# Performance work log

Hardware: AMD Instinct MI355X
Metric: run time of the kernel (lower is better)

Reference implementation:

```python
import jax, jax.numpy as jnp
import numpy as np

D_IN_NUM = 16
D_IN_CAT = 16
D_OUT = 10
DIM = 512
N_FREQ = 32
FREQ_SCALE = 0.01
D_EMB = 48
TEMP = 1.0
CHUNK = 5000


def setup_inputs() -> dict:
    key = jax.random.key(0)
    ks = jax.random.split(key, 10)
    B, N = 1024, 40000
    d_in_total = D_IN_NUM * D_EMB + D_IN_CAT
    return {
        "x_num": jax.random.uniform(ks[0], (B, D_IN_NUM), dtype=jnp.float32),
        "x_cat": jax.random.uniform(ks[1], (B, D_IN_CAT), dtype=jnp.float32),
        "y": jax.random.randint(ks[2], (B,), 0, D_OUT),
        "candidate_x_num": jax.random.uniform(ks[3], (N, D_IN_NUM), dtype=jnp.float32),
        "candidate_x_cat": jax.random.uniform(ks[4], (N, D_IN_CAT), dtype=jnp.float32),
        "candidate_y": jax.random.randint(ks[5], (N,), 0, D_OUT),
        "frequencies": FREQ_SCALE * jax.random.normal(ks[6], (D_IN_NUM, N_FREQ), dtype=jnp.float32),
        "lin_w": 0.05 * jax.random.normal(ks[7], (2 * N_FREQ, D_EMB), dtype=jnp.float32),
        "lin_b": jnp.zeros((D_EMB,), dtype=jnp.float32),
        "enc_w": 0.02 * jax.random.normal(ks[8], (d_in_total, DIM), dtype=jnp.float32),
        "enc_b": jnp.zeros((DIM,), dtype=jnp.float32),
    }


def _plr_encode(x_num, x_cat, frequencies, lin_w, lin_b, enc_w, enc_b):
    # PLR 'lite' embedding: [B, F] -> [B, F, 2*n_freq] -> [B, F, d_emb]
    t = 2.0 * jnp.pi * frequencies[None] * x_num[:, :, None]        # [B,F,n_freq]
    feats = jnp.concatenate([jnp.cos(t), jnp.sin(t)], axis=-1)       # [B,F,2n_freq]
    emb = jax.nn.relu(feats @ lin_w + lin_b)                         # [B,F,d_emb]
    flat = emb.reshape(emb.shape[0], -1)                             # [B,F*d_emb]
    h = jnp.concatenate([flat, x_cat], axis=1) @ enc_w + enc_b       # [B,dim]
    return h


def reference(x_num, x_cat, y, candidate_x_num, candidate_x_cat, candidate_y,
              frequencies, lin_w, lin_b, enc_w, enc_b):
    q = _plr_encode(x_num, x_cat, frequencies, lin_w, lin_b, enc_w, enc_b)           # [B,dim]
    c = _plr_encode(candidate_x_num, candidate_x_cat, frequencies, lin_w, lin_b, enc_w, enc_b)  # [N,dim]
    cand_y = jax.nn.one_hot(candidate_y, D_OUT, dtype=jnp.float32)                   # [N,K]

    # pairwise Euclidean distance (matmul form, as torch.cdist)
    d2 = (jnp.sum(q * q, axis=1, keepdims=True)
          + jnp.sum(c * c, axis=1)[None, :]
          - 2.0 * q @ c.T)
    dist = jnp.sqrt(jnp.maximum(d2, 1e-12)) / TEMP                                   # [B,N]
    exp_d = jnp.exp(-dist)                                                           # [B,N]

    # original accumulates per-5000-chunk logsumexp of exp(-d) additively
    B, N = exp_d.shape
    n_chunks = N // CHUNK
    lse = jax.nn.logsumexp(exp_d.reshape(B, n_chunks, CHUNK), axis=-1).sum(axis=-1)  # [B]
    logits = exp_d @ cand_y                                                          # [B,K]
    return jnp.log(logits) - lse[:, None]
```

## Files before the change

### kernel.cpp

```cpp
#include <hip/hip_runtime.h>
#include <math.h>

typedef __attribute__((ext_vector_type(8))) short bf16x8;
typedef __attribute__((ext_vector_type(4))) float f32x4;
typedef unsigned short u16;
typedef unsigned int u32;

#define BQ 1024
#define NCAND 40000
#define ROWS_TOT 41024
#define NF 16
#define NFREQ 32
#define DEMB 48
#define KDIM 800
#define ASTRIDE 808
#define DIM 512
#define NCLS 10
#define NCHUNK 8
#define CHUNKSZ 5000
#define CT_PER_CHUNK 40
#define NCT 320
#define PSTRIDE 136
#define MROWS 64
#define TWO_PI 6.28318530717958647692f

__device__ __forceinline__ u16 f2bf(float f) {
  u32 u = __float_as_uint(f);
  u32 r = u + 0x7fffu + ((u >> 16) & 1u);
  return (u16)(r >> 16);
}
__device__ __forceinline__ float bf2f(u16 b) { return __uint_as_float(((u32)b) << 16); }
__device__ __forceinline__ u32 cvt_pk_bf16(float lo, float hi) {
  u32 r;
  asm("v_cvt_pk_bf16_f32 %0, %1, %2" : "=v"(r) : "v"(lo), "v"(hi));
  return r;
}

__global__ __launch_bounds__(256)
void k_prep(const float* __restrict__ enc_w, u16* __restrict__ enc_wT)
{
  int idx = blockIdx.x * 256 + threadIdx.x;
  if (idx >= DIM * KDIM) return;
  int n = idx / KDIM, k = idx - n * KDIM;
  u16 v = 0;
  if (k < 784) v = f2bf(enc_w[k * DIM + n]);
  enc_wT[idx] = v;
}

__global__ __launch_bounds__(512, 2)
void k_encode(const float* __restrict__ xq_num, const float* __restrict__ xq_cat,
              const float* __restrict__ xc_num, const float* __restrict__ xc_cat,
              const float* __restrict__ freq, const float* __restrict__ lin_w,
              const float* __restrict__ lin_b, const u16* __restrict__ enc_wT,
              const float* __restrict__ enc_b,
              u16* __restrict__ h_bf, float* __restrict__ norms)
{
  __shared__ u16 a_s[MROWS * ASTRIDE];
  __shared__ float norm_s[MROWS];

  const int t = threadIdx.x;
  const int row0 = blockIdx.x * MROWS;
  const bool isq = (row0 < BQ);
  const float* __restrict__ xnum = isq ? xq_num : xc_num;
  const float* __restrict__ xcat = isq ? xq_cat : xc_cat;
  const int rbase = isq ? row0 : (row0 - BQ);

  const int wid = t >> 6, l = t & 63, hi = l >> 4, lo = l & 15;

  if (t < MROWS) norm_s[t] = 0.f;
  for (int i = t; i < MROWS * 16; i += 512) {
    int r = i >> 4, c = i & 15;
    a_s[r * ASTRIDE + 768 + c] = f2bf(xcat[(rbase + r) * NF + c]);
  }
  for (int i = t; i < MROWS * 24; i += 512) {
    int r = i / 24, c = i - r * 24;
    a_s[r * ASTRIDE + 784 + c] = 0;
  }

  {
    float fq[8];
    *(float4*)&fq[0] = *(const float4*)&freq[lo * NFREQ + hi * 8];
    *(float4*)&fq[4] = *(const float4*)&freq[lo * NFREQ + hi * 8 + 4];
    float xv[8];
#pragma unroll
    for (int mi = 0; mi < 8; ++mi)
      xv[mi] = xnum[(rbase + wid * 8 + mi) * NF + lo];

    bf16x8 lwb[2][3];
#pragma unroll
    for (int kf = 0; kf < 2; ++kf)
#pragma unroll
      for (int nf = 0; nf < 3; ++nf)
#pragma unroll
        for (int e = 0; e < 8; ++e)
          lwb[kf][nf][e] = (short)f2bf(lin_w[(kf * 32 + hi * 8 + e) * DEMB + nf * 16 + lo]);
    float lb[3];
#pragma unroll
    for (int nf = 0; nf < 3; ++nf) lb[nf] = lin_b[nf * 16 + lo];

#pragma unroll
    for (int mi = 0; mi < 8; ++mi) {
      bf16x8 ac, as_;
#pragma unroll
      for (int e = 0; e < 8; ++e) {
        float tt = TWO_PI * fq[e] * xv[mi];
        ac[e] = (short)f2bf(__cosf(tt));
        as_[e] = (short)f2bf(__sinf(tt));
      }
#pragma unroll
      for (int nf = 0; nf < 3; ++nf) {
        f32x4 ec = {0.f, 0.f, 0.f, 0.f};
        ec = __builtin_amdgcn_mfma_f32_16x16x32_bf16(ac, lwb[0][nf], ec, 0, 0, 0);
        ec = __builtin_amdgcn_mfma_f32_16x16x32_bf16(as_, lwb[1][nf], ec, 0, 0, 0);
#pragma unroll
        for (int reg = 0; reg < 4; ++reg) {
          int f = hi * 4 + reg;
          int r = wid * 8 + mi;
          float v = fmaxf(ec[reg] + lb[nf], 0.f);
          a_s[r * ASTRIDE + f * DEMB + nf * 16 + lo] = f2bf(v);
        }
      }
    }
  }
  __syncthreads();

  f32x4 acc[4][4];
#pragma unroll
  for (int mf = 0; mf < 4; ++mf)
#pragma unroll
    for (int nf = 0; nf < 4; ++nf) acc[mf][nf] = 0.f;

  const u16* bwbase = enc_wT + (size_t)(wid * 64 + lo) * KDIM + hi * 8;
  const u16* asbase = a_s + lo * ASTRIDE + hi * 8;

  bf16x8 afA[4], bwA[4], afB[4], bwB[4];

#define LOADK(kt, af, bw)                                                     \
  {                                                                           \
    _Pragma("unroll")                                                         \
    for (int nf = 0; nf < 4; ++nf)                                            \
      bw[nf] = *(const bf16x8*)(bwbase + (size_t)nf * 16 * KDIM + (kt) * 32); \
    _Pragma("unroll")                                                         \
    for (int mf = 0; mf < 4; ++mf)                                            \
      af[mf] = *(const bf16x8*)(asbase + mf * 16 * ASTRIDE + (kt) * 32);      \
  }
#define MFMAK(af, bw)                                                         \
  {                                                                           \
    _Pragma("unroll")                                                         \
    for (int mf = 0; mf < 4; ++mf)                                            \
      _Pragma("unroll")                                                       \
      for (int nf = 0; nf < 4; ++nf)                                          \
        acc[mf][nf] =                                                         \
            __builtin_amdgcn_mfma_f32_16x16x32_bf16(af[mf], bw[nf],           \
                                                    acc[mf][nf], 0, 0, 0);    \
  }

  LOADK(0, afA, bwA);
#pragma unroll
  for (int i = 0; i < 12; ++i) {
    LOADK(2 * i + 1, afB, bwB);
    MFMAK(afA, bwA);
    LOADK(2 * i + 2, afA, bwA);
    MFMAK(afB, bwB);
  }
  MFMAK(afA, bwA);
#undef LOADK
#undef MFMAK

  float encb_v[4];
#pragma unroll
  for (int nf = 0; nf < 4; ++nf) encb_v[nf] = enc_b[wid * 64 + nf * 16 + lo];
  float nacc[4][4];
#pragma unroll
  for (int mf = 0; mf < 4; ++mf)
#pragma unroll
    for (int r = 0; r < 4; ++r) nacc[mf][r] = 0.f;

#pragma unroll
  for (int mf = 0; mf < 4; ++mf)
#pragma unroll
    for (int nf = 0; nf < 4; ++nf)
#pragma unroll
      for (int r = 0; r < 4; ++r) {
        int m = mf * 16 + hi * 4 + r;
        int n = wid * 64 + nf * 16 + lo;
        float hv = acc[mf][nf][r] + encb_v[nf];
        u16 ub = f2bf(hv);
        h_bf[(size_t)(row0 + m) * DIM + n] = ub;
        float hb = bf2f(ub);
        nacc[mf][r] = fmaf(hb, hb, nacc[mf][r]);
      }
#pragma unroll
  for (int mf = 0; mf < 4; ++mf)
#pragma unroll
    for (int r = 0; r < 4; ++r) {
      float v = nacc[mf][r];
      v += __shfl_xor(v, 1); v += __shfl_xor(v, 2);
      v += __shfl_xor(v, 4); v += __shfl_xor(v, 8);
      if (lo == 0) atomicAdd(&norm_s[mf * 16 + hi * 4 + r], v);
    }
  __syncthreads();
  if (t < MROWS) norms[row0 + t] = norm_s[t];
}

__global__ __launch_bounds__(256)
void k_dist(const u16* __restrict__ h_bf, const float* __restrict__ norms,
            const int* __restrict__ cand_y,
            float* __restrict__ cls_part, float* __restrict__ lse_part)
{
  __shared__ __align__(16) u16 AB_s[32768];
  __shared__ float qn_s[128];
  __shared__ float cn_s[128];
  __shared__ int cy_s[128];
  __shared__ float lse_s[128];

  u16* P_s = AB_s;

  const int flat = blockIdx.x;
  const int xcd = flat & 7;
  const int i = flat >> 3;
  const int ct = xcd * CT_PER_CHUNK + (i >> 3);
  const int qt = i & 7;

  const int t = threadIdx.x;
  const int chunk = xcd;
  const int ctl = ct - chunk * CT_PER_CHUNK;
  const int cand0 = chunk * CHUNKSZ + ctl * 128;
  const int cend = chunk * CHUNKSZ + CHUNKSZ;
  const int q0 = qt * 128;

  if (t < 128) {
    lse_s[t] = 0.f;
    qn_s[t] = norms[q0 + t];
    int j = cand0 + t; if (j > cend - 1) j = cend - 1;
    cn_s[t] = norms[BQ + j];
    cy_s[t] = cand_y[j];
  }

  const int wid = t >> 6, l = t & 63, hi = l >> 4, lo = l & 15;
  const int wc = wid & 1, wq = wid >> 1;

#define STAGE(dstoff, kt)                                                      \
  {                                                                            \
    _Pragma("unroll")                                                          \
    for (int p = 0; p < 4; ++p) {                                              \
      int seg = wid * 4 + p;                                                   \
      int lrow = seg * 8 + (l >> 3);                                           \
      int scol = ((l & 7) * 16) ^ ((lrow & 7) << 4);                           \
      int crow = cand0 + lrow; if (crow > cend - 1) crow = cend - 1;           \
      const u16* srcA = h_bf + (size_t)(BQ + crow) * DIM + (kt) * 64 + (scol >> 1); \
      __builtin_amdgcn_global_load_lds(                                        \
          (const __attribute__((address_space(1))) u32*)srcA,                  \
          (__attribute__((address_space(3))) u32*)(AB_s + (dstoff) + seg * 512), \
          16, 0, 0);                                                           \
      const u16* srcB = h_bf + (size_t)(q0 + lrow) * DIM + (kt) * 64 + (scol >> 1); \
      __builtin_amdgcn_global_load_lds(                                        \
          (const __attribute__((address_space(1))) u32*)srcB,                  \
          (__attribute__((address_space(3))) u32*)(AB_s + (dstoff) + 8192 + seg * 512), \
          16, 0, 0);                                                           \
    }                                                                          \
  }

  f32x4 acc[4][4];
#pragma unroll
  for (int mi = 0; mi < 4; ++mi)
#pragma unroll
    for (int ni = 0; ni < 4; ++ni) acc[mi][ni] = 0.f;

  STAGE(0, 0);
  STAGE(16384, 1);

#pragma unroll
  for (int kt = 0; kt < 8; ++kt) {
    if (kt == 7) asm volatile("s_waitcnt vmcnt(0)" ::: "memory");
    else         asm volatile("s_waitcnt vmcnt(8)" ::: "memory");
    __builtin_amdgcn_s_barrier();
    __builtin_amdgcn_sched_barrier(0);

    const u16* Ac = AB_s + (kt & 1) * 16384;
    const u16* Bc = Ac + 8192;
#pragma unroll
    for (int ks = 0; ks < 2; ++ks) {
      bf16x8 af[4], bq[4];
#pragma unroll
      for (int mi = 0; mi < 4; ++mi) {
        int row = wc * 64 + mi * 16 + lo;
        int byt = (hi * 16 + ks * 64) ^ ((row & 7) << 4);
        af[mi] = *(const bf16x8*)&Ac[row * 64 + (byt >> 1)];
      }
#pragma unroll
      for (int ni = 0; ni < 4; ++ni) {
        int row = wq * 64 + ni * 16 + lo;
        int byt = (hi * 16 + ks * 64) ^ ((row & 7) << 4);
        bq[ni] = *(const bf16x8*)&Bc[row * 64 + (byt >> 1)];
      }
#pragma unroll
      for (int mi = 0; mi < 4; ++mi)
#pragma unroll
        for (int ni = 0; ni < 4; ++ni)
          acc[mi][ni] = __builtin_amdgcn_mfma_f32_16x16x32_bf16(af[mi], bq[ni], acc[mi][ni], 0, 0, 0);
    }
    __builtin_amdgcn_sched_barrier(0);
    __builtin_amdgcn_s_barrier();
    if (kt < 6) STAGE((kt & 1) * 16384, kt + 2);
  }
#undef STAGE

  float qv[4];
#pragma unroll
  for (int ni = 0; ni < 4; ++ni) qv[ni] = qn_s[wq * 64 + ni * 16 + lo];

  u32 pk[4][4][2];
  float lacc[4] = {0.f, 0.f, 0.f, 0.f};
#pragma unroll
  for (int mi = 0; mi < 4; ++mi)
#pragma unroll
    for (int ni = 0; ni < 4; ++ni) {
      float ev[4];
#pragma unroll
      for (int r = 0; r < 4; ++r) {
        int crow = wc * 64 + mi * 16 + hi * 4 + r;
        bool valid = (cand0 + crow) < cend;
        float d2 = fmaf(-2.f, acc[mi][ni][r], cn_s[crow] + qv[ni]);
        float dist = __builtin_amdgcn_sqrtf(fmaxf(d2, 1e-12f));
        float e = valid ? __expf(-dist) : 0.f;
        ev[r] = e;
        lacc[ni] += valid ? __expf(e) : 0.f;
      }
      pk[mi][ni][0] = cvt_pk_bf16(ev[0], ev[1]);
      pk[mi][ni][1] = cvt_pk_bf16(ev[2], ev[3]);
    }

#pragma unroll
  for (int ni = 0; ni < 4; ++ni) {
    float v = lacc[ni];
    v += __shfl_xor(v, 16); v += __shfl_xor(v, 32);
    if (hi == 0) atomicAdd(&lse_s[wq * 64 + ni * 16 + lo], v);
  }

  __syncthreads();
#pragma unroll
  for (int mi = 0; mi < 4; ++mi)
#pragma unroll
    for (int ni = 0; ni < 4; ++ni) {
      int q = wq * 64 + ni * 16 + lo;
      int j0 = wc * 64 + mi * 16 + hi * 4;
      *(uint2*)&P_s[q * PSTRIDE + j0] = make_uint2(pk[mi][ni][0], pk[mi][ni][1]);
    }
  __syncthreads();

#pragma unroll
  for (int g = 0; g < 2; ++g) {
    f32x4 accc = {0.f, 0.f, 0.f, 0.f};
    const u16* Prow = P_s + (wid * 32 + g * 16 + lo) * PSTRIDE;
#pragma unroll
    for (int ks = 0; ks < 4; ++ks) {
      bf16x8 af = *(const bf16x8*)(Prow + ks * 32 + hi * 8);
      bf16x8 yb;
#pragma unroll
      for (int e = 0; e < 8; ++e) {
        int j = ks * 32 + hi * 8 + e;
        yb[e] = (short)((cy_s[j] == lo) ? 0x3F80 : 0);
      }
      accc = __builtin_amdgcn_mfma_f32_16x16x32_bf16(af, yb, accc, 0, 0, 0);
    }
    if (lo < NCLS) {
#pragma unroll
      for (int reg = 0; reg < 4; ++reg) {
        int qq = wid * 32 + g * 16 + hi * 4 + reg;
        cls_part[((size_t)ct * BQ + (q0 + qq)) * NCLS + lo] = accc[reg];
      }
    }
  }

  if (t < 128) lse_part[(size_t)ct * BQ + q0 + t] = lse_s[t];
}

__global__ __launch_bounds__(320)
void k_final(const float* __restrict__ cls_part, const float* __restrict__ lse_part,
             float* __restrict__ out)
{
  __shared__ float cls_sum[NCLS];
  __shared__ float ch_sum[NCHUNK];
  const int t = threadIdx.x;
  const int b = blockIdx.x;
  if (t < NCLS) cls_sum[t] = 0.f;
  if (t < NCHUNK) ch_sum[t] = 0.f;
  __syncthreads();

  float cs[NCLS];
#pragma unroll
  for (int c = 0; c < NCLS; ++c) cs[c] = cls_part[((size_t)t * BQ + b) * NCLS + c];
  float ls = lse_part[(size_t)t * BQ + b];
  atomicAdd(&ch_sum[t / CT_PER_CHUNK], ls);
#pragma unroll
  for (int c = 0; c < NCLS; ++c) {
    float w = cs[c];
    w += __shfl_xor(w, 1); w += __shfl_xor(w, 2); w += __shfl_xor(w, 4);
    w += __shfl_xor(w, 8); w += __shfl_xor(w, 16); w += __shfl_xor(w, 32);
    if ((t & 63) == 0) atomicAdd(&cls_sum[c], w);
  }
  __syncthreads();
  if (t < NCLS) {
    float lse = 0.f;
#pragma unroll
    for (int ch = 0; ch < NCHUNK; ++ch) lse += logf(ch_sum[ch]);
    out[b * NCLS + t] = logf(cls_sum[t]) - lse;
  }
}

extern "C" void kernel_launch(void* const* d_in, const int* in_sizes, int n_in,
                              void* d_out, int out_size, void* d_ws, size_t ws_size,
                              hipStream_t stream)
{
  const float* xq_num = (const float*)d_in[0];
  const float* xq_cat = (const float*)d_in[1];
  const float* xc_num = (const float*)d_in[3];
  const float* xc_cat = (const float*)d_in[4];
  const int* cand_y = (const int*)d_in[5];
  const float* freq = (const float*)d_in[6];
  const float* lin_w = (const float*)d_in[7];
  const float* lin_b = (const float*)d_in[8];
  const float* enc_w = (const float*)d_in[9];
  const float* enc_b = (const float*)d_in[10];

  u16* h_bf = (u16*)d_ws;
  float* norms = (float*)((char*)d_ws + (size_t)ROWS_TOT * DIM * 2);
  float* cls_part = norms + ROWS_TOT;
  float* lse_part = cls_part + (size_t)NCT * BQ * NCLS;
  u16* enc_wT = (u16*)(lse_part + (size_t)NCT * BQ);
  float* out = (float*)d_out;

  hipLaunchKernelGGL(k_prep, dim3((DIM * KDIM + 255) / 256), dim3(256), 0, stream,
                     enc_w, enc_wT);
  hipLaunchKernelGGL(k_encode, dim3(ROWS_TOT / MROWS), dim3(512), 0, stream,
                     xq_num, xq_cat, xc_num, xc_cat, freq, lin_w, lin_b,
                     enc_wT, enc_b, h_bf, norms);
  hipLaunchKernelGGL(k_dist, dim3(NCT * 8), dim3(256), 0, stream,
                     h_bf, norms, cand_y, cls_part, lse_part);
  hipLaunchKernelGGL(k_final, dim3(BQ), dim3(320), 0, stream,
                     cls_part, lse_part, out);
}
```

Measured before the change: 179.3 us.

## Tile enc_w transpose via LDS, triple-buffer encode K-loop, raise MFMA priority

The prep kernel now transposes enc_w through a padded 64x65 shared-memory tile, so both global reads and writes are coalesced instead of strided. The encode GEMM loop moves from double to triple buffering with a prefetch distance of two k-steps. Both the encode and distance MFMA sections are wrapped in s_setprio to favour matrix issue. Triple buffering uses more registers, which could reduce occupancy in the 512-thread encode kernel.

```diff
diff --git a/kernel.cpp b/kernel.cpp
--- a/kernel.cpp
+++ b/kernel.cpp
@@ -39,12 +39,25 @@
 __global__ __launch_bounds__(256)
 void k_prep(const float* __restrict__ enc_w, u16* __restrict__ enc_wT)
 {
-  int idx = blockIdx.x * 256 + threadIdx.x;
-  if (idx >= DIM * KDIM) return;
-  int n = idx / KDIM, k = idx - n * KDIM;
-  u16 v = 0;
-  if (k < 784) v = f2bf(enc_w[k * DIM + n]);
-  enc_wT[idx] = v;
+  __shared__ float tile[64][65];
+  const int bk = blockIdx.x % 13;
+  const int bn = blockIdx.x / 13;
+#pragma unroll
+  for (int e = 0; e < 16; ++e) {
+    int r = e * 4 + (threadIdx.x >> 6);
+    int c = threadIdx.x & 63;
+    int k = bk * 64 + r;
+    tile[r][c] = (k < 784) ? enc_w[k * DIM + bn * 64 + c] : 0.f;
+  }
+  __syncthreads();
+#pragma unroll
+  for (int e = 0; e < 16; ++e) {
+    int r = e * 4 + (threadIdx.x >> 6);
+    int c = threadIdx.x & 63;
+    int k = bk * 64 + c;
+    if (k < KDIM)
+      enc_wT[(size_t)(bn * 64 + r) * KDIM + k] = f2bf(tile[c][r]);
+  }
 }
 
 __global__ __launch_bounds__(512, 2)
@@ -133,37 +146,37 @@
   const u16* bwbase = enc_wT + (size_t)(wid * 64 + lo) * KDIM + hi * 8;
   const u16* asbase = a_s + lo * ASTRIDE + hi * 8;
 
-  bf16x8 afA[4], bwA[4], afB[4], bwB[4];
-
-#define LOADK(kt, af, bw)                                                     \
+  bf16x8 afb[3][4], bwb[3][4];
+
+#define LOADK(kt, b)                                                          \
   {                                                                           \
     _Pragma("unroll")                                                         \
     for (int nf = 0; nf < 4; ++nf)                                            \
-      bw[nf] = *(const bf16x8*)(bwbase + (size_t)nf * 16 * KDIM + (kt) * 32); \
+      bwb[b][nf] = *(const bf16x8*)(bwbase + (size_t)nf * 16 * KDIM + (kt) * 32); \
     _Pragma("unroll")                                                         \
     for (int mf = 0; mf < 4; ++mf)                                            \
-      af[mf] = *(const bf16x8*)(asbase + mf * 16 * ASTRIDE + (kt) * 32);      \
-  }
-#define MFMAK(af, bw)                                                         \
+      afb[b][mf] = *(const bf16x8*)(asbase + mf * 16 * ASTRIDE + (kt) * 32);  \
+  }
+#define MFMAK(b)                                                              \
   {                                                                           \
     _Pragma("unroll")                                                         \
     for (int mf = 0; mf < 4; ++mf)                                            \
       _Pragma("unroll")                                                       \
       for (int nf = 0; nf < 4; ++nf)                                          \
         acc[mf][nf] =                                                         \
-            __builtin_amdgcn_mfma_f32_16x16x32_bf16(af[mf], bw[nf],           \
+            __builtin_amdgcn_mfma_f32_16x16x32_bf16(afb[b][mf], bwb[b][nf],   \
                                                     acc[mf][nf], 0, 0, 0);    \
   }
 
-  LOADK(0, afA, bwA);
-#pragma unroll
-  for (int i = 0; i < 12; ++i) {
-    LOADK(2 * i + 1, afB, bwB);
-    MFMAK(afA, bwA);
-    LOADK(2 * i + 2, afA, bwA);
-    MFMAK(afB, bwB);
-  }
-  MFMAK(afA, bwA);
+  LOADK(0, 0);
+  LOADK(1, 1);
+#pragma unroll
+  for (int i = 0; i < 25; ++i) {
+    if (i < 23) LOADK(i + 2, (i + 2) % 3);
+    __builtin_amdgcn_s_setprio(1);
+    MFMAK(i % 3);
+    __builtin_amdgcn_s_setprio(0);
+  }
 #undef LOADK
 #undef MFMAK
 
@@ -279,6 +292,7 @@
 
     const u16* Ac = AB_s + (kt & 1) * 16384;
     const u16* Bc = Ac + 8192;
+    __builtin_amdgcn_s_setprio(1);
 #pragma unroll
     for (int ks = 0; ks < 2; ++ks) {
       bf16x8 af[4], bq[4];
@@ -300,6 +314,7 @@
         for (int ni = 0; ni < 4; ++ni)
           acc[mi][ni] = __builtin_amdgcn_mfma_f32_16x16x32_bf16(af[mi], bq[ni], acc[mi][ni], 0, 0, 0);
     }
+    __builtin_amdgcn_s_setprio(0);
     __builtin_amdgcn_sched_barrier(0);
     __builtin_amdgcn_s_barrier();
     if (kt < 6) STAGE((kt & 1) * 16384, kt + 2);
@@ -431,8 +446,7 @@
   u16* enc_wT = (u16*)(lse_part + (size_t)NCT * BQ);
   float* out = (float*)d_out;
 
-  hipLaunchKernelGGL(k_prep, dim3((DIM * KDIM + 255) / 256), dim3(256), 0, stream,
-                     enc_w, enc_wT);
+  hipLaunchKernelGGL(k_prep, dim3(13 * 8), dim3(256), 0, stream, enc_w, enc_wT);
   hipLaunchKernelGGL(k_encode, dim3(ROWS_TOT / MROWS), dim3(512), 0, stream,
                      xq_num, xq_cat, xc_num, xc_cat, freq, lin_w, lin_b,
                      enc_wT, enc_b, h_bf, norms);
```

After: 182.8 us. Within noise of the previous version (+2.0%).
